# Kernel tuning notes

Hardware: AMD Instinct MI355X
Metric: run time of the kernel (lower is better)

## Reference

```python
import jax, jax.numpy as jnp
import numpy as np

D_MODEL = 1024
N_HEADS = 16


def setup_inputs() -> dict:
    key = jax.random.key(0)
    ks = jax.random.split(key, 5)
    B, T, C = 4, 2048, D_MODEL
    x = jax.random.normal(ks[0], (B, T, C), dtype=jnp.float32)
    s = 1.0 / np.sqrt(C)
    W_attn = jax.random.normal(ks[1], (C, 3 * C), dtype=jnp.float32) * s
    b_attn = jnp.zeros((3 * C,), dtype=jnp.float32)
    W_proj = jax.random.normal(ks[2], (C, C), dtype=jnp.float32) * s
    b_proj = jnp.zeros((C,), dtype=jnp.float32)
    return {"x": x, "W_attn": W_attn, "b_attn": b_attn, "W_proj": W_proj, "b_proj": b_proj}


def reference(x, W_attn, b_attn, W_proj, b_proj):
    B, T, C = x.shape
    H = N_HEADS
    hd = C // H
    qkv = x @ W_attn + b_attn                      # [B,T,3C]
    q, k, v = jnp.split(qkv, 3, axis=-1)
    # reshape to [B,H,T,hd]
    q = q.reshape(B, T, H, hd).transpose(0, 2, 1, 3)
    k = k.reshape(B, T, H, hd).transpose(0, 2, 1, 3)
    v = v.reshape(B, T, H, hd).transpose(0, 2, 1, 3)
    scale = 1.0 / jnp.sqrt(jnp.asarray(hd, dtype=x.dtype))
    aff = jnp.einsum('bhqd,bhkd->bhqk', q, k) * scale   # [B,H,T,T]
    causal = jnp.tril(jnp.ones((T, T), dtype=bool))
    aff = jnp.where(causal, aff, jnp.asarray(-jnp.inf, dtype=aff.dtype))
    p = jax.nn.softmax(aff, axis=-1)
    y = jnp.einsum('bhqk,bhkd->bhqd', p, v)             # [B,H,T,hd]
    y = y.transpose(0, 2, 1, 3).reshape(B, T, C)
    return y @ W_proj + b_proj
```

## Files before the change

### kernel.cpp

```cpp
#include <hip/hip_runtime.h>
#include <stdint.h>
#include <math.h>

typedef __attribute__((ext_vector_type(8))) __bf16 bf16x8;
typedef __attribute__((ext_vector_type(4))) __bf16 bf16x4;
typedef __attribute__((ext_vector_type(4))) float f32x4;
typedef __attribute__((ext_vector_type(16))) float f32x16;

#define MFMA16(A, B, C) __builtin_amdgcn_mfma_f32_16x16x32_bf16((A), (B), (C), 0, 0, 0)
#define MFMA32(A, B, C) __builtin_amdgcn_mfma_f32_32x32x16_bf16((A), (B), (C), 0, 0, 0)

#if defined(__has_builtin)
#if __has_builtin(__builtin_amdgcn_exp2f)
#define EXP2(x) __builtin_amdgcn_exp2f(x)
#else
#define EXP2(x) exp2f(x)
#endif
#else
#define EXP2(x) exp2f(x)
#endif

static constexpr int kT  = 2048;
static constexpr int kC  = 1024;
static constexpr int kHD = 64;
#define QSCALE 0.1803368801111204f

__device__ __forceinline__ void g2l16(const void* g, void* l) {
  __builtin_amdgcn_global_load_lds(
      (const __attribute__((address_space(1))) uint32_t*)g,
      (__attribute__((address_space(3))) uint32_t*)l, 16, 0, 0);
}

__global__ __launch_bounds__(256) void k_prep(const float* __restrict__ x,
                                              __bf16* __restrict__ xb,
                                              const float* __restrict__ Wa,
                                              __bf16* __restrict__ wab,
                                              const float* __restrict__ Wp,
                                              __bf16* __restrict__ wpb) {
  const int bid = (int)blockIdx.x;
  const int tid = threadIdx.x;
  if (bid < 8192) {
    int i = (bid * 256 + tid) * 4;
    f32x4 v = *(const f32x4*)(x + i);
    bf16x4 o;
    o[0] = (__bf16)v[0]; o[1] = (__bf16)v[1]; o[2] = (__bf16)v[2]; o[3] = (__bf16)v[3];
    *(bf16x4*)(xb + i) = o;
    return;
  }
  __shared__ float t[32][33];
  int tb = bid - 8192;
  const float* src; __bf16* dst; int N;
  if (tb < 3072) { src = Wa; dst = wab; N = 3072; }
  else           { tb -= 3072; src = Wp; dst = wpb; N = 1024; }
  const int k0 = (tb & 31) * 32, n0 = (tb >> 5) * 32;
  const int c = tid & 31, r = tid >> 5;
#pragma unroll
  for (int i = 0; i < 4; ++i)
    t[r + i * 8][c] = src[(size_t)(k0 + r + i * 8) * N + n0 + c];
  __syncthreads();
#pragma unroll
  for (int i = 0; i < 4; ++i)
    dst[(size_t)(n0 + r + i * 8) * 1024 + k0 + c] = (__bf16)t[c][r + i * 8];
}

static constexpr int GK = 1024;
static constexpr int GNT = GK / 32;

template <int MODE>
__global__ __launch_bounds__(256, 3) void k_gemm(const __bf16* __restrict__ A,
                                                 const __bf16* __restrict__ Bw,
                                                 const float* __restrict__ bias,
                                                 __bf16* __restrict__ qo,
                                                 __bf16* __restrict__ ko,
                                                 __bf16* __restrict__ vo,
                                                 float* __restrict__ out) {
  __shared__ __bf16 As[3][128 * 32];
  __shared__ __bf16 Bs[3][128 * 32];

  const int tid = threadIdx.x;
  const int wave = tid >> 6, lane = tid & 63;
  const int lo = lane & 15, hi = lane >> 4;
  const int wr = wave & 1, wc = wave >> 1;

  constexpr int NBN = (MODE == 0) ? 24 : 8;
  const int nwg = (int)gridDim.x;
  const int id = (int)blockIdx.x;
  const int wg = (id & 7) * (nwg >> 3) + (id >> 3);
  const int bm = wg / NBN, bn = wg % NBN;
  const int m0 = bm * 128, n0 = bn * 128;

  const int rG0 = tid >> 2, gG0 = (tid & 3) ^ ((rG0 >> 1) & 3);
  const int rG1 = (tid + 256) >> 2, gG1 = ((tid + 256) & 3) ^ ((rG1 >> 1) & 3);
  const __bf16* gaA0 = A + (size_t)(m0 + rG0) * GK + gG0 * 8;
  const __bf16* gaA1 = A + (size_t)(m0 + rG1) * GK + gG1 * 8;
  const __bf16* gbB0 = Bw + (size_t)(n0 + rG0) * GK + gG0 * 8;
  const __bf16* gbB1 = Bw + (size_t)(n0 + rG1) * GK + gG1 * 8;

  const int fsw = (hi ^ ((lo >> 1) & 3)) * 8;
  const int offA = (wr * 64 + lo) * 32 + fsw;
  const int offB = (wc * 64 + lo) * 32 + fsw;

  f32x4 acc[4][4] = {};

#define GSTAGE(jt, bufi)                                  \
  {                                                       \
    g2l16(gaA0 + (jt) * 32, &As[(bufi)][tid * 8]);        \
    g2l16(gaA1 + (jt) * 32, &As[(bufi)][2048 + tid * 8]); \
    g2l16(gbB0 + (jt) * 32, &Bs[(bufi)][tid * 8]);        \
    g2l16(gbB1 + (jt) * 32, &Bs[(bufi)][2048 + tid * 8]); \
  }

#define GMFMA(RB)                                                            \
  {                                                                          \
    bf16x8 af[4], bfr[4];                                                    \
    _Pragma("unroll")                                                        \
    for (int m = 0; m < 4; ++m)                                              \
      af[m] = *(const bf16x8*)&As[RB][offA + m * 512];                       \
    _Pragma("unroll")                                                        \
    for (int n = 0; n < 4; ++n)                                              \
      bfr[n] = *(const bf16x8*)&Bs[RB][offB + n * 512];                      \
    __builtin_amdgcn_s_setprio(1);                                           \
    _Pragma("unroll")                                                        \
    for (int m = 0; m < 4; ++m)                                              \
      _Pragma("unroll")                                                      \
      for (int n = 0; n < 4; ++n)                                            \
        acc[m][n] = MFMA16(af[m], bfr[n], acc[m][n]);                        \
    __builtin_amdgcn_s_setprio(0);                                           \
  }

#define GITER(RB, RS, JT)                            \
  {                                                  \
    GSTAGE((JT) + 2, RS);                            \
    GMFMA(RB);                                       \
    asm volatile("s_waitcnt vmcnt(4)" ::: "memory"); \
    __builtin_amdgcn_s_barrier();                    \
    __builtin_amdgcn_sched_barrier(0);               \
  }

  GSTAGE(0, 0);
  GSTAGE(1, 1);
  asm volatile("s_waitcnt vmcnt(4)" ::: "memory");
  __builtin_amdgcn_s_barrier();
  __builtin_amdgcn_sched_barrier(0);

#pragma unroll 1
  for (int j = 0; j < GNT - 2; j += 3) {
    GITER(0, 2, j);
    GITER(1, 0, j + 1);
    GITER(2, 1, j + 2);
  }
  GMFMA(0);
  asm volatile("s_waitcnt vmcnt(0)" ::: "memory");
  __builtin_amdgcn_s_barrier();
  __builtin_amdgcn_sched_barrier(0);
  GMFMA(1);

#undef GITER
#undef GMFMA
#undef GSTAGE

  if (MODE == 0) {
#pragma unroll
    for (int nj = 0; nj < 4; ++nj) {
      int gn = n0 + wc * 64 + nj * 16 + lo;
      float bv = bias[gn];
      int which = gn >> 10;
      int c = gn & 1023;
      int hh = c >> 6, d = c & 63;
#pragma unroll
      for (int mi = 0; mi < 4; ++mi) {
        int gm = m0 + wr * 64 + mi * 16 + hi * 4;
        int bb = gm >> 11, t0 = gm & 2047;
        if (which == 2) {
          int t0p = t0 ^ ((((t0 >> 2) ^ (t0 >> 3)) & 1) * 12);
          bf16x4 vv;
#pragma unroll
          for (int r = 0; r < 4; ++r) vv[r] = (__bf16)(acc[mi][nj][r] + bv);
          *(bf16x4*)(vo + ((size_t)(bb * 16 + hh) * 64 + d) * 2048 + t0p) = vv;
        } else {
#pragma unroll
          for (int r = 0; r < 4; ++r) {
            float val = acc[mi][nj][r] + bv;
            size_t idx = (((size_t)(bb * 16 + hh)) * 2048 + (t0 + r)) * 64 + d;
            if (which == 0)
              qo[idx] = (__bf16)(val * QSCALE);
            else
              ko[idx] = (__bf16)val;
          }
        }
      }
    }
  } else {
#pragma unroll
    for (int nj = 0; nj < 4; ++nj) {
      int gn = n0 + wc * 64 + nj * 16 + lo;
      float bv = bias[gn];
#pragma unroll
      for (int mi = 0; mi < 4; ++mi) {
        int gm = m0 + wr * 64 + mi * 16 + hi * 4;
#pragma unroll
        for (int r = 0; r < 4; ++r)
          out[(size_t)(gm + r) * 1024 + gn] = acc[mi][nj][r] + bv;
      }
    }
  }
}

__global__ __launch_bounds__(256, 2) void k_flash(const __bf16* __restrict__ qb,
                                                  const __bf16* __restrict__ kb,
                                                  const __bf16* __restrict__ vt,
                                                  __bf16* __restrict__ ob) {
  __shared__ __bf16 Ks[3][64 * 64];
  __shared__ __bf16 Vs[3][64 * 64];

  const int id = (int)blockIdx.x;
  const int xcd = id & 7, jj = id >> 3;
  const int bh = (jj & 7) * 8 + xcd;
  const int xsi = jj >> 3;
  const int xs = (xsi < 4) ? xsi : 11 - xsi;
  const int b = bh >> 4, h = bh & 15;
  const int tid = threadIdx.x, wave = tid >> 6, lane = tid & 63;
  const int l31 = lane & 31, hi32 = lane >> 5;
  const int gx = l31 & 7;

  const int qrow[2] = { (15 - xs) * 128 + wave * 32, xs * 128 + wave * 32 };

  bf16x8 qf[2][4];
#pragma unroll
  for (int rg = 0; rg < 2; ++rg) {
    const __bf16* Qp = qb + ((size_t)bh * kT + qrow[rg] + l31) * kHD + hi32 * 8;
#pragma unroll
    for (int ks = 0; ks < 4; ++ks)
      qf[rg][ks] = *(const bf16x8*)(Qp + ks * 16);
  }

  f32x16 acc[2][2] = {};
  float srow[2] = {0.0f, 0.0f};

  const __bf16* Kbase = kb + (size_t)bh * kT * kHD;
  const __bf16* Vbase = vt + (size_t)bh * kHD * kT;

  int srcK[2], srcV[2];
#pragma unroll
  for (int p = 0; p < 2; ++p) {
    int g = wave * 64 + lane + p * 256;
    int r = g >> 3, c = g & 7;
    int cs = c ^ (r & 7);
    srcK[p] = r * kHD + cs * 8;
    srcV[p] = r * kT + cs * 8;
  }

  const int nt = 32 - 2 * xs;

#pragma unroll
  for (int p = 0; p < 2; ++p) {
    g2l16(Kbase + srcK[p], &Ks[0][wave * 512 + p * 2048]);
    g2l16(Vbase + srcV[p], &Vs[0][wave * 512 + p * 2048]);
  }
#pragma unroll
  for (int p = 0; p < 2; ++p) {
    g2l16(Kbase + 64 * kHD + srcK[p], &Ks[1][wave * 512 + p * 2048]);
    g2l16(Vbase + 64 + srcV[p],       &Vs[1][wave * 512 + p * 2048]);
  }
  asm volatile("s_waitcnt vmcnt(4)" ::: "memory");
  __builtin_amdgcn_s_barrier();
  __builtin_amdgcn_sched_barrier(0);

  int rb = 0, rs = 2;
  for (int it = 0; it < nt; ++it) {
    const int kt = it * 64;
    const bool both = (it <= 2 * xs + 1);

    if (it + 2 < nt) {
      const int kn = kt + 128;
#pragma unroll
      for (int p = 0; p < 2; ++p) {
        g2l16(Kbase + kn * kHD + srcK[p], &Ks[rs][wave * 512 + p * 2048]);
        g2l16(Vbase + kn + srcV[p],       &Vs[rs][wave * 512 + p * 2048]);
      }
    }

    const __bf16* Kt = &Ks[rb][0];
    const __bf16* Vt = &Vs[rb][0];

    bf16x8 pa[2][4];

#pragma unroll
    for (int kb2 = 0; kb2 < 2; ++kb2) {
      bf16x8 ka[4];
#pragma unroll
      for (int ks = 0; ks < 4; ++ks)
        ka[ks] = *(const bf16x8*)&Kt[(kb2 * 32 + l31) * 64 +
                                     (((ks * 2 + hi32) ^ gx) * 8)];
#pragma unroll
      for (int rg = 0; rg < 2; ++rg) {
        if (rg == 1 && !both) break;
        f32x16 s = {};
        __builtin_amdgcn_s_setprio(1);
#pragma unroll
        for (int ks = 0; ks < 4; ++ks) s = MFMA32(ka[ks], qf[rg][ks], s);
        __builtin_amdgcn_s_setprio(0);
        const int qg = qrow[rg] + l31;
        const int kbs = kt + kb2 * 32 + 4 * hi32;
        if (kt + kb2 * 32 + 31 > qrow[rg]) {
#pragma unroll
          for (int i = 0; i < 16; ++i)
            if (kbs + (i & 3) + 8 * (i >> 2) > qg) s[i] = -INFINITY;
        }
#pragma unroll
        for (int i = 0; i < 16; ++i) s[i] = EXP2(s[i]);
        float sm = 0.0f;
#pragma unroll
        for (int i = 0; i < 16; ++i) sm += s[i];
        srow[rg] += sm;
#pragma unroll
        for (int a = 0; a < 2; ++a) {
          bf16x8 p;
#pragma unroll
          for (int e = 0; e < 8; ++e) p[e] = (__bf16)s[8 * a + e];
          pa[rg][kb2 * 2 + a] = p;
        }
      }
    }

    __builtin_amdgcn_s_setprio(1);
#pragma unroll
    for (int db = 0; db < 2; ++db) {
#pragma unroll
      for (int ks = 0; ks < 4; ++ks) {
        bf16x8 vb = *(const bf16x8*)&Vt[(db * 32 + l31) * 64 +
                                        (((ks * 2 + hi32) ^ gx) * 8)];
        acc[0][db] = MFMA32(pa[0][ks], vb, acc[0][db]);
        if (both) acc[1][db] = MFMA32(pa[1][ks], vb, acc[1][db]);
      }
    }
    __builtin_amdgcn_s_setprio(0);

    if (it + 2 < nt) {
      asm volatile("s_waitcnt vmcnt(4)" ::: "memory");
    } else if (it + 2 == nt) {
      asm volatile("s_waitcnt vmcnt(0)" ::: "memory");
    }
    if (it + 1 < nt) {
      __builtin_amdgcn_s_barrier();
      __builtin_amdgcn_sched_barrier(0);
    }
    rb = (rb == 2) ? 0 : rb + 1;
    rs = (rs == 2) ? 0 : rs + 1;
  }

#pragma unroll
  for (int rg = 0; rg < 2; ++rg) {
    float tot = srow[rg] + __shfl_xor(srow[rg], 32, 64);
    float invt = 1.0f / tot;
    __bf16* Op = ob + ((size_t)b * kT + qrow[rg]) * kC + h * kHD;
#pragma unroll
    for (int i = 0; i < 16; ++i) {
      int q = (i & 3) + 8 * (i >> 2) + 4 * hi32;
      float inv = __shfl(invt, q, 64);
      Op[(size_t)q * kC + l31]      = (__bf16)(acc[rg][0][i] * inv);
      Op[(size_t)q * kC + 32 + l31] = (__bf16)(acc[rg][1][i] * inv);
    }
  }
}

extern "C" void kernel_launch(void* const* d_in, const int* in_sizes, int n_in,
                              void* d_out, int out_size, void* d_ws, size_t ws_size,
                              hipStream_t stream) {
  const float* x      = (const float*)d_in[0];
  const float* W_attn = (const float*)d_in[1];
  const float* b_attn = (const float*)d_in[2];
  const float* W_proj = (const float*)d_in[3];
  const float* b_proj = (const float*)d_in[4];
  float* out = (float*)d_out;

  char* ws = (char*)d_ws;
  __bf16* xb  = (__bf16*)(ws + 0);
  __bf16* ob  = (__bf16*)(ws + 0);
  __bf16* wab = (__bf16*)(ws + 16777216);
  __bf16* wpb = (__bf16*)(ws + 23068672);
  __bf16* qbf = (__bf16*)(ws + 25165824);
  __bf16* kbf = (__bf16*)(ws + 41943040);
  __bf16* vtb = (__bf16*)(ws + 58720256);

  k_prep<<<12288, 256, 0, stream>>>(x, xb, W_attn, wab, W_proj, wpb);
  k_gemm<0><<<dim3(1536), 256, 0, stream>>>(xb, wab, b_attn, qbf, kbf, vtb, nullptr);
  k_flash<<<dim3(512), 256, 0, stream>>>(qbf, kbf, vtb, ob);
  k_gemm<1><<<dim3(512), 256, 0, stream>>>(ob, wpb, b_proj, nullptr, nullptr, nullptr, out);
}
```

Before: 237.7 us.

## Split QKV GEMM into 256x256-tile, 8-wave kernel with interleaved LDS staging

The QKV projection GEMM moves from a 128x128 tile with 4 waves and K-step 32 to a 256x256 tile with 8 waves, K-step 64 and double-buffered LDS. Global-to-LDS loads are interleaved between four MFMA quadrants, with barriers and priority hints. The larger tile raises arithmetic intensity and cuts global/L2 traffic for the largest GEMM. The costs are 384 blocks, which may fill the CUs less evenly, and heavy register and LDS use, 128KB per block. The output projection GEMM is split into its own specialised kernel with a hard-coded grid mapping.

```diff
diff --git a/kernel.cpp b/kernel.cpp
--- a/kernel.cpp
+++ b/kernel.cpp
@@ -66,14 +66,188 @@
 static constexpr int GK = 1024;
 static constexpr int GNT = GK / 32;
 
-template <int MODE>
-__global__ __launch_bounds__(256, 3) void k_gemm(const __bf16* __restrict__ A,
-                                                 const __bf16* __restrict__ Bw,
-                                                 const float* __restrict__ bias,
-                                                 __bf16* __restrict__ qo,
-                                                 __bf16* __restrict__ ko,
-                                                 __bf16* __restrict__ vo,
-                                                 float* __restrict__ out) {
+__global__ __launch_bounds__(512, 2) void k_gemm_qkv(const __bf16* __restrict__ A,
+                                                     const __bf16* __restrict__ Bw,
+                                                     const float* __restrict__ bias,
+                                                     __bf16* __restrict__ qo,
+                                                     __bf16* __restrict__ ko,
+                                                     __bf16* __restrict__ vo) {
+  __shared__ __bf16 As[2][2][128 * 64];
+  __shared__ __bf16 Bs[2][2][128 * 64];
+
+  const int tid = threadIdx.x;
+  const int wid = tid >> 6, lane = tid & 63;
+  const int lo = lane & 15, hi = lane >> 4;
+  const int wr = wid >> 2, wc = wid & 3;
+  const int bhalf = wc >> 1;
+
+  const int id = (int)blockIdx.x;
+  const int wg = (id & 7) * 48 + (id >> 3);
+  const int bm = wg / 12, bn = wg % 12;
+  const int m0 = bm * 256, n0 = bn * 256;
+
+  const int srow = tid >> 3;
+  const int scs = (tid & 7) ^ (srow & 7);
+  const __bf16* gA = A + (size_t)(m0 + srow) * GK + scs * 8;
+  const __bf16* gB = Bw + (size_t)(n0 + srow) * GK + scs * 8;
+
+#define STG_A(kt, hf, bufi)                                                  \
+  {                                                                          \
+    g2l16(gA + (size_t)((hf) * 128) * GK + (kt) * 64,                        \
+          &As[bufi][hf][tid * 8]);                                           \
+    g2l16(gA + (size_t)((hf) * 128 + 64) * GK + (kt) * 64,                   \
+          &As[bufi][hf][4096 + tid * 8]);                                    \
+  }
+#define STG_B(kt, hf, bufi)                                                  \
+  {                                                                          \
+    g2l16(gB + (size_t)((hf) * 128) * GK + (kt) * 64,                        \
+          &Bs[bufi][hf][tid * 8]);                                           \
+    g2l16(gB + (size_t)((hf) * 128 + 64) * GK + (kt) * 64,                   \
+          &Bs[bufi][hf][4096 + tid * 8]);                                    \
+  }
+
+  const int gxl = lo & 7;
+  const int arow = lo * 64;
+  const int brow = ((wc & 1) * 64 + lo) * 64;
+  int kofs[2];
+#pragma unroll
+  for (int kk = 0; kk < 2; ++kk) kofs[kk] = (((kk << 2) + hi) ^ gxl) * 8;
+
+  f32x4 acc[8][4] = {};
+
+  STG_A(0, 0, 0); STG_A(0, 1, 0); STG_B(0, 0, 0); STG_B(0, 1, 0);
+  STG_A(1, 0, 1); STG_A(1, 1, 1);
+  asm volatile("s_waitcnt vmcnt(4)" ::: "memory");
+  __builtin_amdgcn_s_barrier();
+  __builtin_amdgcn_sched_barrier(0);
+
+#pragma unroll 2
+  for (int k = 0; k < 16; ++k) {
+    const int cbuf = k & 1, nbuf = cbuf ^ 1;
+    bf16x8 aL[4][2], aH[4][2], bL[2][2], bH[2][2];
+
+#pragma unroll
+    for (int mi = 0; mi < 4; ++mi)
+#pragma unroll
+      for (int kk = 0; kk < 2; ++kk)
+        aL[mi][kk] = *(const bf16x8*)&As[cbuf][wr][arow + mi * 1024 + kofs[kk]];
+#pragma unroll
+    for (int nj = 0; nj < 2; ++nj)
+#pragma unroll
+      for (int kk = 0; kk < 2; ++kk)
+        bL[nj][kk] = *(const bf16x8*)&Bs[cbuf][bhalf][brow + nj * 1024 + kofs[kk]];
+    if (k + 1 < 16) STG_B(k + 1, 0, nbuf);
+    __builtin_amdgcn_s_barrier();
+    __builtin_amdgcn_s_setprio(1);
+#pragma unroll
+    for (int mi = 0; mi < 4; ++mi)
+#pragma unroll
+      for (int nj = 0; nj < 2; ++nj)
+#pragma unroll
+        for (int kk = 0; kk < 2; ++kk)
+          acc[mi][nj] = MFMA16(aL[mi][kk], bL[nj][kk], acc[mi][nj]);
+    __builtin_amdgcn_s_setprio(0);
+    __builtin_amdgcn_s_barrier();
+    __builtin_amdgcn_sched_barrier(0);
+
+#pragma unroll
+    for (int mi = 0; mi < 4; ++mi)
+#pragma unroll
+      for (int kk = 0; kk < 2; ++kk)
+        aH[mi][kk] = *(const bf16x8*)&As[cbuf][wr][arow + (mi + 4) * 1024 + kofs[kk]];
+    if (k + 1 < 16) STG_B(k + 1, 1, nbuf);
+    __builtin_amdgcn_s_barrier();
+    __builtin_amdgcn_s_setprio(1);
+#pragma unroll
+    for (int mi = 0; mi < 4; ++mi)
+#pragma unroll
+      for (int nj = 0; nj < 2; ++nj)
+#pragma unroll
+        for (int kk = 0; kk < 2; ++kk)
+          acc[mi + 4][nj] = MFMA16(aH[mi][kk], bL[nj][kk], acc[mi + 4][nj]);
+    __builtin_amdgcn_s_setprio(0);
+    __builtin_amdgcn_s_barrier();
+    __builtin_amdgcn_sched_barrier(0);
+
+#pragma unroll
+    for (int nj = 0; nj < 2; ++nj)
+#pragma unroll
+      for (int kk = 0; kk < 2; ++kk)
+        bH[nj][kk] = *(const bf16x8*)&Bs[cbuf][bhalf][brow + (nj + 2) * 1024 + kofs[kk]];
+    if (k + 2 < 16) STG_A(k + 2, 0, cbuf);
+    __builtin_amdgcn_s_barrier();
+    __builtin_amdgcn_s_setprio(1);
+#pragma unroll
+    for (int mi = 0; mi < 4; ++mi)
+#pragma unroll
+      for (int nj = 0; nj < 2; ++nj)
+#pragma unroll
+        for (int kk = 0; kk < 2; ++kk)
+          acc[mi][nj + 2] = MFMA16(aL[mi][kk], bH[nj][kk], acc[mi][nj + 2]);
+    __builtin_amdgcn_s_setprio(0);
+    __builtin_amdgcn_s_barrier();
+    __builtin_amdgcn_sched_barrier(0);
+
+    if (k + 2 < 16) STG_A(k + 2, 1, cbuf);
+    __builtin_amdgcn_s_barrier();
+    __builtin_amdgcn_s_setprio(1);
+#pragma unroll
+    for (int mi = 0; mi < 4; ++mi)
+#pragma unroll
+      for (int nj = 0; nj < 2; ++nj)
+#pragma unroll
+        for (int kk = 0; kk < 2; ++kk)
+          acc[mi + 4][nj + 2] = MFMA16(aH[mi][kk], bH[nj][kk], acc[mi + 4][nj + 2]);
+    __builtin_amdgcn_s_setprio(0);
+    if (k <= 13) {
+      asm volatile("s_waitcnt vmcnt(4)" ::: "memory");
+    } else if (k == 14) {
+      asm volatile("s_waitcnt vmcnt(0)" ::: "memory");
+    }
+    if (k < 15) {
+      __builtin_amdgcn_s_barrier();
+      __builtin_amdgcn_sched_barrier(0);
+    }
+  }
+#undef STG_A
+#undef STG_B
+
+#pragma unroll
+  for (int nj = 0; nj < 4; ++nj) {
+    int gn = n0 + wc * 64 + nj * 16 + lo;
+    float bv = bias[gn];
+    int which = gn >> 10;
+    int c = gn & 1023;
+    int hh = c >> 6, d = c & 63;
+#pragma unroll
+    for (int mi = 0; mi < 8; ++mi) {
+      int gm = m0 + wr * 128 + mi * 16 + hi * 4;
+      int bb = gm >> 11, t0 = gm & 2047;
+      if (which == 2) {
+        int t0p = t0 ^ ((((t0 >> 2) ^ (t0 >> 3)) & 1) * 12);
+        bf16x4 vv;
+#pragma unroll
+        for (int r = 0; r < 4; ++r) vv[r] = (__bf16)(acc[mi][nj][r] + bv);
+        *(bf16x4*)(vo + ((size_t)(bb * 16 + hh) * 64 + d) * 2048 + t0p) = vv;
+      } else {
+#pragma unroll
+        for (int r = 0; r < 4; ++r) {
+          float val = acc[mi][nj][r] + bv;
+          size_t idx = (((size_t)(bb * 16 + hh)) * 2048 + (t0 + r)) * 64 + d;
+          if (which == 0)
+            qo[idx] = (__bf16)(val * QSCALE);
+          else
+            ko[idx] = (__bf16)val;
+        }
+      }
+    }
+  }
+}
+
+__global__ __launch_bounds__(256, 3) void k_gemm_proj(const __bf16* __restrict__ A,
+                                                      const __bf16* __restrict__ Bw,
+                                                      const float* __restrict__ bias,
+                                                      float* __restrict__ out) {
   __shared__ __bf16 As[3][128 * 32];
   __shared__ __bf16 Bs[3][128 * 32];
 
@@ -82,11 +256,9 @@
   const int lo = lane & 15, hi = lane >> 4;
   const int wr = wave & 1, wc = wave >> 1;
 
-  constexpr int NBN = (MODE == 0) ? 24 : 8;
-  const int nwg = (int)gridDim.x;
   const int id = (int)blockIdx.x;
-  const int wg = (id & 7) * (nwg >> 3) + (id >> 3);
-  const int bm = wg / NBN, bn = wg % NBN;
+  const int wg = (id & 7) * 64 + (id >> 3);
+  const int bm = wg / 8, bn = wg % 8;
   const int m0 = bm * 128, n0 = bn * 128;
 
   const int rG0 = tid >> 2, gG0 = (tid & 3) ^ ((rG0 >> 1) & 3);
@@ -159,49 +331,16 @@
 #undef GMFMA
 #undef GSTAGE
 
-  if (MODE == 0) {
-#pragma unroll
-    for (int nj = 0; nj < 4; ++nj) {
-      int gn = n0 + wc * 64 + nj * 16 + lo;
-      float bv = bias[gn];
-      int which = gn >> 10;
-      int c = gn & 1023;
-      int hh = c >> 6, d = c & 63;
-#pragma unroll
-      for (int mi = 0; mi < 4; ++mi) {
-        int gm = m0 + wr * 64 + mi * 16 + hi * 4;
-        int bb = gm >> 11, t0 = gm & 2047;
-        if (which == 2) {
-          int t0p = t0 ^ ((((t0 >> 2) ^ (t0 >> 3)) & 1) * 12);
-          bf16x4 vv;
-#pragma unroll
-          for (int r = 0; r < 4; ++r) vv[r] = (__bf16)(acc[mi][nj][r] + bv);
-          *(bf16x4*)(vo + ((size_t)(bb * 16 + hh) * 64 + d) * 2048 + t0p) = vv;
-        } else {
-#pragma unroll
-          for (int r = 0; r < 4; ++r) {
-            float val = acc[mi][nj][r] + bv;
-            size_t idx = (((size_t)(bb * 16 + hh)) * 2048 + (t0 + r)) * 64 + d;
-            if (which == 0)
-              qo[idx] = (__bf16)(val * QSCALE);
-            else
-              ko[idx] = (__bf16)val;
-          }
-        }
-      }
-    }
-  } else {
-#pragma unroll
-    for (int nj = 0; nj < 4; ++nj) {
-      int gn = n0 + wc * 64 + nj * 16 + lo;
-      float bv = bias[gn];
-#pragma unroll
-      for (int mi = 0; mi < 4; ++mi) {
-        int gm = m0 + wr * 64 + mi * 16 + hi * 4;
-#pragma unroll
-        for (int r = 0; r < 4; ++r)
-          out[(size_t)(gm + r) * 1024 + gn] = acc[mi][nj][r] + bv;
-      }
+#pragma unroll
+  for (int nj = 0; nj < 4; ++nj) {
+    int gn = n0 + wc * 64 + nj * 16 + lo;
+    float bv = bias[gn];
+#pragma unroll
+    for (int mi = 0; mi < 4; ++mi) {
+      int gm = m0 + wr * 64 + mi * 16 + hi * 4;
+#pragma unroll
+      for (int r = 0; r < 4; ++r)
+        out[(size_t)(gm + r) * 1024 + gn] = acc[mi][nj][r] + bv;
     }
   }
 }
@@ -384,7 +523,7 @@
   __bf16* vtb = (__bf16*)(ws + 58720256);
 
   k_prep<<<12288, 256, 0, stream>>>(x, xb, W_attn, wab, W_proj, wpb);
-  k_gemm<0><<<dim3(1536), 256, 0, stream>>>(xb, wab, b_attn, qbf, kbf, vtb, nullptr);
+  k_gemm_qkv<<<dim3(384), 512, 0, stream>>>(xb, wab, b_attn, qbf, kbf, vtb);
   k_flash<<<dim3(512), 256, 0, stream>>>(qbf, kbf, vtb, ob);
-  k_gemm<1><<<dim3(512), 256, 0, stream>>>(ob, wpb, b_proj, nullptr, nullptr, nullptr, out);
+  k_gemm_proj<<<dim3(512), 256, 0, stream>>>(ob, wpb, b_proj, out);
 }
```

Result: slower. 251.3 us (+5.7%).
